# Kernel optimization log

Hardware: AMD Instinct MI355X
Metric: run time of the kernel (lower is better)

## Reference

```python
import jax, jax.numpy as jnp
import numpy as np
import math

N_HEAD = 16
ROPE_BASE = 10000.0


def _rotate_half(x):
    d2 = x.shape[-1] // 2
    return jnp.concatenate([-x[..., d2:], x[..., :d2]], axis=-1)


def _rope_sin_cos(T, d_head, dtype):
    half = d_head // 2
    inv_freq = ROPE_BASE ** (-(jnp.arange(half, dtype=dtype) / half))  # (half,)
    t = jnp.arange(T, dtype=dtype)[:, None]                            # (T,1)
    angles = t * inv_freq[None, :]                                     # (T,half)
    sin = jnp.sin(angles)
    cos = jnp.cos(angles)
    sin = jnp.concatenate([sin, sin], axis=-1)  # (T,d_head)
    cos = jnp.concatenate([cos, cos], axis=-1)
    return sin, cos


def setup_inputs() -> dict:
    key = jax.random.key(0)
    ks = jax.random.split(key, 4)
    B, T, C = 2, 2048, 1024
    x = jax.random.normal(ks[0], (B, T, C), dtype=jnp.float32)
    padding_mask = jnp.ones((B, T), dtype=bool)
    W_kqv = jax.random.normal(ks[1], (3 * C, C), dtype=jnp.float32) * (1.0 / math.sqrt(C))
    b_kqv = jnp.zeros((3 * C,), dtype=jnp.float32)
    W_proj = jax.random.normal(ks[2], (C, C), dtype=jnp.float32) * (1.0 / math.sqrt(C))
    b_proj = jnp.zeros((C,), dtype=jnp.float32)
    return {"x": x, "padding_mask": padding_mask, "W_kqv": W_kqv,
            "b_kqv": b_kqv, "W_proj": W_proj, "b_proj": b_proj}


def reference(x, padding_mask, W_kqv, b_kqv, W_proj, b_proj):
    B, T, C = x.shape
    H = N_HEAD
    D = C // H
    qkv = jnp.einsum('btc,fc->btf', x, W_kqv) + b_kqv  # (B,T,3C)
    # NOTE: original chunks as k, q, v (in that order)
    k, q, v = jnp.split(qkv, 3, axis=-1)

    def split_heads(t):
        return t.reshape(B, T, H, D).transpose(0, 2, 1, 3)  # (B,H,T,D)

    q, k, v = split_heads(q), split_heads(k), split_heads(v)

    sin, cos = _rope_sin_cos(T, D, x.dtype)  # (T,D)
    sin = sin[None, None]
    cos = cos[None, None]
    q = q * cos + _rotate_half(q) * sin
    k = k * cos + _rotate_half(k) * sin

    att = jnp.einsum('bhqd,bhkd->bhqk', q, k) * (1.0 / math.sqrt(D))  # (B,H,T,T)
    causal = jnp.tril(jnp.ones((T, T), dtype=bool))[None, None]
    att = jnp.where(causal, att, -jnp.inf)
    key_mask = padding_mask[:, None, None, :]
    att = jnp.where(key_mask, att, -jnp.inf)
    att = jax.nn.softmax(att, axis=-1)
    y = jnp.einsum('bhqk,bhkd->bhqd', att, v)  # (B,H,T,D)
    qry_mask = padding_mask[:, None, :, None].astype(y.dtype)
    y = y * qry_mask
    y = y.transpose(0, 2, 1, 3).reshape(B, T, C)
    return jnp.einsum('btc,oc->bto', y, W_proj) + b_proj
```

## Files before the change

### kernel.cpp

```cpp
#include <hip/hip_runtime.h>

typedef unsigned short u16;
typedef unsigned int   u32;
typedef __attribute__((ext_vector_type(4))) float f32x4;
typedef __attribute__((ext_vector_type(2))) float f32x2;
typedef __attribute__((ext_vector_type(8))) short short8;
typedef __attribute__((ext_vector_type(8))) unsigned short u16x8;
typedef __attribute__((ext_vector_type(4))) unsigned short u16x4;
typedef __attribute__((ext_vector_type(2))) unsigned int u32x2;

__device__ __forceinline__ u16 f2b(float f) {
  u32 u = __float_as_uint(f);
  u32 r = u + 0x7FFFu + ((u >> 16) & 1u);
  return (u16)(r >> 16);
}

__device__ __forceinline__ void gl_lds16(const void* g, void* l) {
  __builtin_amdgcn_global_load_lds((const __attribute__((address_space(1))) void*)g,
                                   (__attribute__((address_space(3))) void*)l, 16, 0, 0);
}

__global__ void cvt_all(const float* __restrict__ x, const float* __restrict__ wk,
                        const float* __restrict__ wp,
                        u16* __restrict__ xb, u16* __restrict__ wkb, u16* __restrict__ wpb,
                        float* __restrict__ cs) {
  if (blockIdx.x >= 8192) {
    const int t = (blockIdx.x - 8192) * 8 + (threadIdx.x >> 5);
    const int i = threadIdx.x & 31;
    float inv = powf(10000.0f, -((float)i) / 32.0f);
    float ang = (float)t * inv;
    f32x2 p; p[0] = cosf(ang); p[1] = sinf(ang);
    *(f32x2*)&cs[t * 64 + i * 2] = p;
    return;
  }
  int i = blockIdx.x * 256 + threadIdx.x;
  const float* s; u16* d; int off;
  if (i < 1048576)      { s = x;  d = xb;  off = i; }
  else if (i < 1835008) { s = wk; d = wkb; off = i - 1048576; }
  else                  { s = wp; d = wpb; off = i - 1835008; }
  f32x4 v = ((const f32x4*)s)[off];
  u16x4 o;
#pragma unroll
  for (int j = 0; j < 4; ++j) o[j] = f2b(v[j]);
  ((u16x4*)d)[off] = o;
}

template <int OUT_BF16>
__global__ __launch_bounds__(256, 3) void gemm_bt(
    const u16* __restrict__ A, const u16* __restrict__ Bt,
    const float* __restrict__ bias, void* __restrict__ Cv,
    int M, int N, int K) {
  __shared__ __align__(16) u16 As[128 * 64];
  __shared__ __align__(16) u16 Bs[128 * 64];
  const int tid = threadIdx.x;
  const int lane = tid & 63;
  const int w = tid >> 6;
  const int wr = w >> 1, wc = w & 1;
  const int l15 = lane & 15, l4 = lane >> 4;
  const int ntn = N >> 7;
  const int bm = blockIdx.x / ntn;
  const int bn = blockIdx.x - bm * ntn;
  const int m0 = bm << 7, n0 = bn << 7;

  int rc[4], so[4];
#pragma unroll
  for (int j = 0; j < 4; ++j) {
    const int c = tid + j * 256;
    rc[j] = c >> 3;
    so[j] = ((c & 7) ^ (rc[j] & 7)) << 3;
  }
  const int sw = l15 & 7;

  f32x4 acc[4][4] = {};

  for (int kt = 0; kt < K; kt += 64) {
    __syncthreads();
#pragma unroll
    for (int j = 0; j < 4; ++j) {
      gl_lds16(A + (size_t)(m0 + rc[j]) * K + kt + so[j], &As[(tid + j * 256) * 8]);
      gl_lds16(Bt + (size_t)(n0 + rc[j]) * K + kt + so[j], &Bs[(tid + j * 256) * 8]);
    }
    __syncthreads();
    short8 af[4][2], bf[4][2];
#pragma unroll
    for (int m = 0; m < 4; ++m)
#pragma unroll
      for (int kk = 0; kk < 2; ++kk)
        af[m][kk] = *(const short8*)&As[(wr * 64 + m * 16 + l15) * 64 + (((kk * 4 + l4) ^ sw) << 3)];
#pragma unroll
    for (int n = 0; n < 4; ++n)
#pragma unroll
      for (int kk = 0; kk < 2; ++kk)
        bf[n][kk] = *(const short8*)&Bs[(wc * 64 + n * 16 + l15) * 64 + (((kk * 4 + l4) ^ sw) << 3)];
#pragma unroll
    for (int m = 0; m < 4; ++m)
#pragma unroll
      for (int n = 0; n < 4; ++n) {
        acc[m][n] = __builtin_amdgcn_mfma_f32_16x16x32_bf16(af[m][0], bf[n][0], acc[m][n], 0, 0, 0);
        acc[m][n] = __builtin_amdgcn_mfma_f32_16x16x32_bf16(af[m][1], bf[n][1], acc[m][n], 0, 0, 0);
      }
  }

#pragma unroll
  for (int n = 0; n < 4; ++n) {
    const int col = n0 + wc * 64 + n * 16 + l15;
    const float bv = bias[col];
#pragma unroll
    for (int m = 0; m < 4; ++m) {
      const int row0 = m0 + wr * 64 + m * 16 + l4 * 4;
#pragma unroll
      for (int r = 0; r < 4; ++r) {
        float v = acc[m][n][r] + bv;
        if (OUT_BF16)
          ((u16*)Cv)[(size_t)(row0 + r) * N + col] = f2b(v);
        else
          ((float*)Cv)[(size_t)(row0 + r) * N + col] = v;
      }
    }
  }
}

__global__ __launch_bounds__(256, 3) void gemm_qkv(
    const u16* __restrict__ A, const u16* __restrict__ Bt,
    const float* __restrict__ bias, const float* __restrict__ cs,
    u16* __restrict__ qb, u16* __restrict__ kb, u16* __restrict__ vT) {
  const int K = 1024;
  __shared__ __align__(16) u16 As[128 * 64];
  __shared__ __align__(16) u16 Bs[128 * 64];
  const int tid = threadIdx.x;
  const int lane = tid & 63;
  const int w = tid >> 6;
  const int wr = w >> 1, wc = w & 1;
  const int l15 = lane & 15, l4 = lane >> 4;
  const int ntn = 24;
  const int bm = blockIdx.x / ntn;
  const int bn = blockIdx.x - bm * ntn;
  const int m0 = bm << 7, n0 = bn << 7;

  int rc[4], so[4];
#pragma unroll
  for (int j = 0; j < 4; ++j) {
    const int c = tid + j * 256;
    rc[j] = c >> 3;
    so[j] = ((c & 7) ^ (rc[j] & 7)) << 3;
  }
  const int sw = l15 & 7;

  f32x4 acc[4][4] = {};

  for (int kt = 0; kt < K; kt += 64) {
    __syncthreads();
#pragma unroll
    for (int j = 0; j < 4; ++j) {
      gl_lds16(A + (size_t)(m0 + rc[j]) * K + kt + so[j], &As[(tid + j * 256) * 8]);
      gl_lds16(Bt + (size_t)(n0 + rc[j]) * K + kt + so[j], &Bs[(tid + j * 256) * 8]);
    }
    __syncthreads();
    short8 af[4][2], bf[4][2];
#pragma unroll
    for (int m = 0; m < 4; ++m)
#pragma unroll
      for (int kk = 0; kk < 2; ++kk)
        af[m][kk] = *(const short8*)&As[(wr * 64 + m * 16 + l15) * 64 + (((kk * 4 + l4) ^ sw) << 3)];
#pragma unroll
    for (int n = 0; n < 4; ++n)
#pragma unroll
      for (int kk = 0; kk < 2; ++kk)
        bf[n][kk] = *(const short8*)&Bs[(wc * 64 + n * 16 + l15) * 64 + (((kk * 4 + l4) ^ sw) << 3)];
#pragma unroll
    for (int m = 0; m < 4; ++m)
#pragma unroll
      for (int n = 0; n < 4; ++n) {
        acc[m][n] = __builtin_amdgcn_mfma_f32_16x16x32_bf16(af[m][0], bf[n][0], acc[m][n], 0, 0, 0);
        acc[m][n] = __builtin_amdgcn_mfma_f32_16x16x32_bf16(af[m][1], bf[n][1], acc[m][n], 0, 0, 0);
      }
  }

  const int hb = bn * 2 + wc;
  const int f = hb >> 4;
  const int head = hb & 15;

  if (f == 2) {
#pragma unroll
    for (int n = 0; n < 4; ++n) {
      const int d = n * 16 + l15;
      const float bv = bias[hb * 64 + d];
#pragma unroll
      for (int m = 0; m < 4; ++m) {
        const int row = m0 + wr * 64 + m * 16 + l4 * 4;
        const int b = row >> 11, t0 = row & 2047;
        u16x4 pk;
#pragma unroll
        for (int r = 0; r < 4; ++r) pk[r] = f2b(acc[m][n][r] + bv);
        *(u16x4*)&vT[((size_t)((b * 16 + head) * 64 + d)) * 2048 + t0] = pk;
      }
    }
  } else {
    u16* const dst = (f == 1) ? qb : kb;
    const float qs = (f == 1) ? 0.180336881f : 1.0f;
#pragma unroll
    for (int n = 0; n < 2; ++n) {
      const int d = n * 16 + l15;
      const float blo = bias[hb * 64 + d];
      const float bhi = bias[hb * 64 + d + 32];
#pragma unroll
      for (int m = 0; m < 4; ++m) {
        const int row = m0 + wr * 64 + m * 16 + l4 * 4;
        const int b = row >> 11, t0 = row & 2047;
        const size_t base = ((size_t)((b * 16 + head) * 2048 + t0)) * 64 + 2 * d;
#pragma unroll
        for (int r = 0; r < 4; ++r) {
          const f32x2 csv = *(const f32x2*)&cs[(size_t)(t0 + r) * 64 + d * 2];
          const float lo = acc[m][n][r] + blo;
          const float hi = acc[m][n + 2][r] + bhi;
          const float olo = (lo * csv[0] - hi * csv[1]) * qs;
          const float ohi = (hi * csv[0] + lo * csv[1]) * qs;
          u32 pw;
          asm("v_cvt_pk_bf16_f32 %0, %1, %2" : "=v"(pw) : "v"(olo), "v"(ohi));
          *(u32*)&dst[base + (size_t)r * 64] = pw;
        }
      }
    }
  }
}

__device__ __forceinline__ void attn9_step(
    const u16* __restrict__ Kp, const u16* __restrict__ Vp,
    u32* __restrict__ P, int kv0, int q0w, bool masked, int l15, int l4,
    const short8& qf0, const short8& qf1, f32x4 (&acc)[4], float& rs) {
  f32x4 st[4];
  __builtin_amdgcn_s_setprio(1);
#pragma unroll
  for (int nb = 0; nb < 4; ++nb) {
    const int rr = nb * 16 + l15;
    const int e0 = (l4 ^ (rr & 7)) << 3;
    const int e1 = ((l4 + 4) ^ (rr & 7)) << 3;
    const short8 k0 = *(const short8*)&Kp[rr * 64 + e0];
    const short8 k1 = *(const short8*)&Kp[rr * 64 + e1];
    f32x4 a = {};
    a = __builtin_amdgcn_mfma_f32_16x16x32_bf16(k0, qf0, a, 0, 0, 0);
    a = __builtin_amdgcn_mfma_f32_16x16x32_bf16(k1, qf1, a, 0, 0, 0);
    st[nb] = a;
  }
  __builtin_amdgcn_s_setprio(0);
  const int qq = q0w + l15;
  float rsl = 0.f;
#pragma unroll
  for (int nb = 0; nb < 4; ++nb) {
    float p[4];
#pragma unroll
    for (int r = 0; r < 4; ++r) {
      float s = st[nb][r];
      const int kk = kv0 + nb * 16 + l4 * 4 + r;
      s = (masked && (kk > qq)) ? -1e30f : s;
      asm("v_exp_f32 %0, %1" : "=v"(p[r]) : "v"(s));
      rsl += p[r];
    }
    u32x2 pw;
    asm("v_cvt_pk_bf16_f32 %0, %1, %2" : "=v"(pw[0]) : "v"(p[0]), "v"(p[1]));
    asm("v_cvt_pk_bf16_f32 %0, %1, %2" : "=v"(pw[1]) : "v"(p[2]), "v"(p[3]));
    *(u32x2*)&P[l15 * 36 + nb * 8 + l4 * 2] = pw;
  }
  rs += rsl;
  const short8 pa0 = *(const short8*)&P[l15 * 36 + l4 * 4];
  const short8 pa1 = *(const short8*)&P[l15 * 36 + 16 + l4 * 4];
  __builtin_amdgcn_s_setprio(1);
#pragma unroll
  for (int dnb = 0; dnb < 4; ++dnb) {
    const int rr = dnb * 16 + l15;
    const int e0 = (l4 ^ (rr & 7)) << 3;
    const int e1 = ((l4 + 4) ^ (rr & 7)) << 3;
    const short8 v0 = *(const short8*)&Vp[rr * 64 + e0];
    const short8 v1 = *(const short8*)&Vp[rr * 64 + e1];
    acc[dnb] = __builtin_amdgcn_mfma_f32_16x16x32_bf16(pa0, v0, acc[dnb], 0, 0, 0);
    acc[dnb] = __builtin_amdgcn_mfma_f32_16x16x32_bf16(pa1, v1, acc[dnb], 0, 0, 0);
  }
  __builtin_amdgcn_s_setprio(0);
}

__global__ __launch_bounds__(256, 3) void attn9(
    const u16* __restrict__ qb, const u16* __restrict__ kb,
    const u16* __restrict__ vT, u16* __restrict__ yb) {
  __shared__ __align__(16) u16 Ks[2][64 * 64];
  __shared__ __align__(16) u16 Vs[2][64 * 64];
  __shared__ __align__(16) u32 Psm[4][16 * 36];
  const int tid = threadIdx.x;
  const int lane = tid & 63;
  const int w = tid >> 6;
  const int l15 = lane & 15, l4 = lane >> 4;
  const int bh = blockIdx.x & 31;
  const int qi = 31 - (blockIdx.x >> 5);
  const int b = bh >> 4, head = bh & 15;
  const int p0 = qi * 64;
  const int nst = qi + 1;
  const int q0w = p0 + w * 16;

  const u16* qbase = qb + (size_t)bh * 2048 * 64;
  const u16* kbase = kb + (size_t)bh * 2048 * 64;
  const u16* vbase = vT + (size_t)bh * 64 * 2048;
  u32* const P = &Psm[w][0];

  const int r0 = tid >> 3, c0 = tid & 7;
  const int r1 = (tid + 256) >> 3, c1 = tid & 7;
  const int sc0 = ((c0 ^ (r0 & 7)) << 3);
  const int sc1 = ((c1 ^ (r1 & 7)) << 3);
  u16* const Kd0 = &Ks[0][tid * 8];        u16* const Kd0b = &Ks[0][(tid + 256) * 8];
  u16* const Kd1 = &Ks[1][tid * 8];        u16* const Kd1b = &Ks[1][(tid + 256) * 8];
  u16* const Vd0 = &Vs[0][tid * 8];        u16* const Vd0b = &Vs[0][(tid + 256) * 8];
  u16* const Vd1 = &Vs[1][tid * 8];        u16* const Vd1b = &Vs[1][(tid + 256) * 8];

#define STAGE(BUF, KV0)                                                        \
  do {                                                                         \
    const int _kv = (KV0);                                                     \
    gl_lds16(kbase + (size_t)(_kv + r0) * 64 + sc0, (BUF) ? Kd1 : Kd0);        \
    gl_lds16(kbase + (size_t)(_kv + r1) * 64 + sc1, (BUF) ? Kd1b : Kd0b);      \
    gl_lds16(vbase + (size_t)r0 * 2048 + _kv + sc0, (BUF) ? Vd1 : Vd0);        \
    gl_lds16(vbase + (size_t)r1 * 2048 + _kv + sc1, (BUF) ? Vd1b : Vd0b);      \
  } while (0)

  const short8 qf0 = *(const short8*)&qbase[(size_t)(q0w + l15) * 64 + l4 * 8];
  const short8 qf1 = *(const short8*)&qbase[(size_t)(q0w + l15) * 64 + 32 + l4 * 8];
  f32x4 acc[4] = {};
  float rs = 0.f;

  int cur = 0;
  STAGE(0, 0);
  for (int t = 0; t < nst; ++t) {
    __syncthreads();
    if (t + 1 < nst) STAGE(cur ^ 1, (t + 1) * 64);
    attn9_step(&Ks[cur][0], &Vs[cur][0], P, t * 64, q0w, t == nst - 1,
               l15, l4, qf0, qf1, acc, rs);
    cur ^= 1;
  }
#undef STAGE

  float rsum = rs;
  rsum += __shfl_xor(rsum, 16);
  rsum += __shfl_xor(rsum, 32);
  float linv[4];
#pragma unroll
  for (int r = 0; r < 4; ++r) linv[r] = 1.f / __shfl(rsum, l4 * 4 + r);
#pragma unroll
  for (int dnb = 0; dnb < 4; ++dnb) {
    const int col = head * 64 + dnb * 16 + l15;
#pragma unroll
    for (int r = 0; r < 4; ++r) {
      const int q = q0w + l4 * 4 + r;
      yb[((size_t)(b * 2048 + q)) * 1024 + col] = f2b(acc[dnb][r] * linv[r]);
    }
  }
}

extern "C" void kernel_launch(void* const* d_in, const int* in_sizes, int n_in,
                              void* d_out, int out_size, void* d_ws, size_t ws_size,
                              hipStream_t stream) {
  const float* x = (const float*)d_in[0];
  const float* W_kqv = (const float*)d_in[2];
  const float* b_kqv = (const float*)d_in[3];
  const float* W_proj = (const float*)d_in[4];
  const float* b_proj = (const float*)d_in[5];
  float* out = (float*)d_out;
  char* ws = (char*)d_ws;
  const size_t MB = (size_t)1 << 20;
  u16* xb = (u16*)(ws + 0);
  u16* wkb = (u16*)(ws + 8 * MB);
  u16* wpb = (u16*)(ws + 14 * MB);
  u16* qb = (u16*)(ws + 40 * MB);
  u16* kb = (u16*)(ws + 48 * MB);
  u16* vTb = (u16*)(ws + 56 * MB);
  u16* yb = (u16*)(ws + 64 * MB);
  float* cs = (float*)(ws + 72 * MB);

  cvt_all<<<8448, 256, 0, stream>>>(x, W_kqv, W_proj, xb, wkb, wpb, cs);
  gemm_qkv<<<768, 256, 0, stream>>>(xb, wkb, b_kqv, cs, qb, kb, vTb);
  attn9<<<1024, 256, 0, stream>>>(qb, kb, vTb, yb);
  gemm_bt<0><<<256, 256, 0, stream>>>(yb, wpb, b_proj, out, 4096, 1024, 1024);
}
```

Before: 104.2 us.

## Process two query sub-tiles per wave in attention, halving waves per block

The attention kernel now uses 2 waves per block instead of 4, and each wave handles 32 query rows as two 16-row halves. Each K/V fragment read from shared memory is reused for both halves, which halves LDS read traffic per MFMA. The cost is more registers per wave, fewer waves per block to hide latency, and each thread issuing twice as many global-to-LDS copies per stage.

```diff
diff --git a/kernel.cpp b/kernel.cpp
--- a/kernel.cpp
+++ b/kernel.cpp
@@ -224,11 +224,12 @@
   }
 }
 
-__device__ __forceinline__ void attn9_step(
+__device__ __forceinline__ void attn10_step(
     const u16* __restrict__ Kp, const u16* __restrict__ Vp,
-    u32* __restrict__ P, int kv0, int q0w, bool masked, int l15, int l4,
-    const short8& qf0, const short8& qf1, f32x4 (&acc)[4], float& rs) {
-  f32x4 st[4];
+    u32* __restrict__ P0, u32* __restrict__ P1,
+    int kv0, int q0w, bool masked, int l15, int l4,
+    const short8 (&qf)[2][2], f32x4 (&acc)[2][4], float (&rs)[2]) {
+  f32x4 st[2][4];
   __builtin_amdgcn_s_setprio(1);
 #pragma unroll
   for (int nb = 0; nb < 4; ++nb) {
@@ -237,33 +238,42 @@
     const int e1 = ((l4 + 4) ^ (rr & 7)) << 3;
     const short8 k0 = *(const short8*)&Kp[rr * 64 + e0];
     const short8 k1 = *(const short8*)&Kp[rr * 64 + e1];
-    f32x4 a = {};
-    a = __builtin_amdgcn_mfma_f32_16x16x32_bf16(k0, qf0, a, 0, 0, 0);
-    a = __builtin_amdgcn_mfma_f32_16x16x32_bf16(k1, qf1, a, 0, 0, 0);
-    st[nb] = a;
+    f32x4 a0 = {}, a1 = {};
+    a0 = __builtin_amdgcn_mfma_f32_16x16x32_bf16(k0, qf[0][0], a0, 0, 0, 0);
+    a0 = __builtin_amdgcn_mfma_f32_16x16x32_bf16(k1, qf[0][1], a0, 0, 0, 0);
+    a1 = __builtin_amdgcn_mfma_f32_16x16x32_bf16(k0, qf[1][0], a1, 0, 0, 0);
+    a1 = __builtin_amdgcn_mfma_f32_16x16x32_bf16(k1, qf[1][1], a1, 0, 0, 0);
+    st[0][nb] = a0;
+    st[1][nb] = a1;
   }
   __builtin_amdgcn_s_setprio(0);
-  const int qq = q0w + l15;
-  float rsl = 0.f;
-#pragma unroll
-  for (int nb = 0; nb < 4; ++nb) {
-    float p[4];
-#pragma unroll
-    for (int r = 0; r < 4; ++r) {
-      float s = st[nb][r];
-      const int kk = kv0 + nb * 16 + l4 * 4 + r;
-      s = (masked && (kk > qq)) ? -1e30f : s;
-      asm("v_exp_f32 %0, %1" : "=v"(p[r]) : "v"(s));
-      rsl += p[r];
-    }
-    u32x2 pw;
-    asm("v_cvt_pk_bf16_f32 %0, %1, %2" : "=v"(pw[0]) : "v"(p[0]), "v"(p[1]));
-    asm("v_cvt_pk_bf16_f32 %0, %1, %2" : "=v"(pw[1]) : "v"(p[2]), "v"(p[3]));
-    *(u32x2*)&P[l15 * 36 + nb * 8 + l4 * 2] = pw;
-  }
-  rs += rsl;
-  const short8 pa0 = *(const short8*)&P[l15 * 36 + l4 * 4];
-  const short8 pa1 = *(const short8*)&P[l15 * 36 + 16 + l4 * 4];
+#pragma unroll
+  for (int h = 0; h < 2; ++h) {
+    u32* const P = h ? P1 : P0;
+    const int qq = q0w + h * 16 + l15;
+    float rsl = 0.f;
+#pragma unroll
+    for (int nb = 0; nb < 4; ++nb) {
+      float p[4];
+#pragma unroll
+      for (int r = 0; r < 4; ++r) {
+        float s = st[h][nb][r];
+        const int kk = kv0 + nb * 16 + l4 * 4 + r;
+        s = (masked && (kk > qq)) ? -1e30f : s;
+        asm("v_exp_f32 %0, %1" : "=v"(p[r]) : "v"(s));
+        rsl += p[r];
+      }
+      u32x2 pw;
+      asm("v_cvt_pk_bf16_f32 %0, %1, %2" : "=v"(pw[0]) : "v"(p[0]), "v"(p[1]));
+      asm("v_cvt_pk_bf16_f32 %0, %1, %2" : "=v"(pw[1]) : "v"(p[2]), "v"(p[3]));
+      *(u32x2*)&P[l15 * 36 + nb * 8 + l4 * 2] = pw;
+    }
+    rs[h] += rsl;
+  }
+  const short8 pa00 = *(const short8*)&P0[l15 * 36 + l4 * 4];
+  const short8 pa01 = *(const short8*)&P0[l15 * 36 + 16 + l4 * 4];
+  const short8 pa10 = *(const short8*)&P1[l15 * 36 + l4 * 4];
+  const short8 pa11 = *(const short8*)&P1[l15 * 36 + 16 + l4 * 4];
   __builtin_amdgcn_s_setprio(1);
 #pragma unroll
   for (int dnb = 0; dnb < 4; ++dnb) {
@@ -272,18 +282,20 @@
     const int e1 = ((l4 + 4) ^ (rr & 7)) << 3;
     const short8 v0 = *(const short8*)&Vp[rr * 64 + e0];
     const short8 v1 = *(const short8*)&Vp[rr * 64 + e1];
-    acc[dnb] = __builtin_amdgcn_mfma_f32_16x16x32_bf16(pa0, v0, acc[dnb], 0, 0, 0);
-    acc[dnb] = __builtin_amdgcn_mfma_f32_16x16x32_bf16(pa1, v1, acc[dnb], 0, 0, 0);
+    acc[0][dnb] = __builtin_amdgcn_mfma_f32_16x16x32_bf16(pa00, v0, acc[0][dnb], 0, 0, 0);
+    acc[0][dnb] = __builtin_amdgcn_mfma_f32_16x16x32_bf16(pa01, v1, acc[0][dnb], 0, 0, 0);
+    acc[1][dnb] = __builtin_amdgcn_mfma_f32_16x16x32_bf16(pa10, v0, acc[1][dnb], 0, 0, 0);
+    acc[1][dnb] = __builtin_amdgcn_mfma_f32_16x16x32_bf16(pa11, v1, acc[1][dnb], 0, 0, 0);
   }
   __builtin_amdgcn_s_setprio(0);
 }
 
-__global__ __launch_bounds__(256, 3) void attn9(
+__global__ __launch_bounds__(128, 2) void attn10(
     const u16* __restrict__ qb, const u16* __restrict__ kb,
     const u16* __restrict__ vT, u16* __restrict__ yb) {
   __shared__ __align__(16) u16 Ks[2][64 * 64];
   __shared__ __align__(16) u16 Vs[2][64 * 64];
-  __shared__ __align__(16) u32 Psm[4][16 * 36];
+  __shared__ __align__(16) u32 Psm[2][2][16 * 36];
   const int tid = threadIdx.x;
   const int lane = tid & 63;
   const int w = tid >> 6;
@@ -293,60 +305,68 @@
   const int b = bh >> 4, head = bh & 15;
   const int p0 = qi * 64;
   const int nst = qi + 1;
-  const int q0w = p0 + w * 16;
+  const int q0w = p0 + w * 32;
 
   const u16* qbase = qb + (size_t)bh * 2048 * 64;
   const u16* kbase = kb + (size_t)bh * 2048 * 64;
   const u16* vbase = vT + (size_t)bh * 64 * 2048;
-  u32* const P = &Psm[w][0];
-
-  const int r0 = tid >> 3, c0 = tid & 7;
-  const int r1 = (tid + 256) >> 3, c1 = tid & 7;
-  const int sc0 = ((c0 ^ (r0 & 7)) << 3);
-  const int sc1 = ((c1 ^ (r1 & 7)) << 3);
-  u16* const Kd0 = &Ks[0][tid * 8];        u16* const Kd0b = &Ks[0][(tid + 256) * 8];
-  u16* const Kd1 = &Ks[1][tid * 8];        u16* const Kd1b = &Ks[1][(tid + 256) * 8];
-  u16* const Vd0 = &Vs[0][tid * 8];        u16* const Vd0b = &Vs[0][(tid + 256) * 8];
-  u16* const Vd1 = &Vs[1][tid * 8];        u16* const Vd1b = &Vs[1][(tid + 256) * 8];
-
-#define STAGE(BUF, KV0)                                                        \
-  do {                                                                         \
-    const int _kv = (KV0);                                                     \
-    gl_lds16(kbase + (size_t)(_kv + r0) * 64 + sc0, (BUF) ? Kd1 : Kd0);        \
-    gl_lds16(kbase + (size_t)(_kv + r1) * 64 + sc1, (BUF) ? Kd1b : Kd0b);      \
-    gl_lds16(vbase + (size_t)r0 * 2048 + _kv + sc0, (BUF) ? Vd1 : Vd0);        \
-    gl_lds16(vbase + (size_t)r1 * 2048 + _kv + sc1, (BUF) ? Vd1b : Vd0b);      \
+  u32* const P0 = &Psm[w][0][0];
+  u32* const P1 = &Psm[w][1][0];
+
+  int rc[4], sc[4];
+#pragma unroll
+  for (int j = 0; j < 4; ++j) {
+    const int c = tid + j * 128;
+    rc[j] = c >> 3;
+    sc[j] = ((c & 7) ^ (rc[j] & 7)) << 3;
+  }
+
+#define STAGE(BUF, KV0)                                                         \
+  do {                                                                          \
+    const int _kv = (KV0);                                                      \
+    _Pragma("unroll")                                                           \
+    for (int j = 0; j < 4; ++j) {                                               \
+      gl_lds16(kbase + (size_t)(_kv + rc[j]) * 64 + sc[j], &Ks[BUF][(tid + j * 128) * 8]); \
+      gl_lds16(vbase + (size_t)rc[j] * 2048 + _kv + sc[j], &Vs[BUF][(tid + j * 128) * 8]); \
+    }                                                                           \
   } while (0)
 
-  const short8 qf0 = *(const short8*)&qbase[(size_t)(q0w + l15) * 64 + l4 * 8];
-  const short8 qf1 = *(const short8*)&qbase[(size_t)(q0w + l15) * 64 + 32 + l4 * 8];
-  f32x4 acc[4] = {};
-  float rs = 0.f;
+  short8 qf[2][2];
+#pragma unroll
+  for (int h = 0; h < 2; ++h) {
+    qf[h][0] = *(const short8*)&qbase[(size_t)(q0w + h * 16 + l15) * 64 + l4 * 8];
+    qf[h][1] = *(const short8*)&qbase[(size_t)(q0w + h * 16 + l15) * 64 + 32 + l4 * 8];
+  }
+  f32x4 acc[2][4] = {};
+  float rs[2] = {0.f, 0.f};
 
   int cur = 0;
   STAGE(0, 0);
   for (int t = 0; t < nst; ++t) {
     __syncthreads();
     if (t + 1 < nst) STAGE(cur ^ 1, (t + 1) * 64);
-    attn9_step(&Ks[cur][0], &Vs[cur][0], P, t * 64, q0w, t == nst - 1,
-               l15, l4, qf0, qf1, acc, rs);
+    attn10_step(&Ks[cur][0], &Vs[cur][0], P0, P1, t * 64, q0w, t == nst - 1,
+                l15, l4, qf, acc, rs);
     cur ^= 1;
   }
 #undef STAGE
 
-  float rsum = rs;
-  rsum += __shfl_xor(rsum, 16);
-  rsum += __shfl_xor(rsum, 32);
-  float linv[4];
-#pragma unroll
-  for (int r = 0; r < 4; ++r) linv[r] = 1.f / __shfl(rsum, l4 * 4 + r);
-#pragma unroll
-  for (int dnb = 0; dnb < 4; ++dnb) {
-    const int col = head * 64 + dnb * 16 + l15;
-#pragma unroll
-    for (int r = 0; r < 4; ++r) {
-      const int q = q0w + l4 * 4 + r;
-      yb[((size_t)(b * 2048 + q)) * 1024 + col] = f2b(acc[dnb][r] * linv[r]);
+#pragma unroll
+  for (int h = 0; h < 2; ++h) {
+    float rsum = rs[h];
+    rsum += __shfl_xor(rsum, 16);
+    rsum += __shfl_xor(rsum, 32);
+    float linv[4];
+#pragma unroll
+    for (int r = 0; r < 4; ++r) linv[r] = 1.f / __shfl(rsum, l4 * 4 + r);
+#pragma unroll
+    for (int dnb = 0; dnb < 4; ++dnb) {
+      const int col = head * 64 + dnb * 16 + l15;
+#pragma unroll
+      for (int r = 0; r < 4; ++r) {
+        const int q = q0w + h * 16 + l4 * 4 + r;
+        yb[((size_t)(b * 2048 + q)) * 1024 + col] = f2b(acc[h][dnb][r] * linv[r]);
+      }
     }
   }
 }
@@ -373,6 +393,6 @@
 
   cvt_all<<<8448, 256, 0, stream>>>(x, W_kqv, W_proj, xb, wkb, wpb, cs);
   gemm_qkv<<<768, 256, 0, stream>>>(xb, wkb, b_kqv, cs, qb, kb, vTb);
-  attn9<<<1024, 256, 0, stream>>>(qb, kb, vTb, yb);
+  attn10<<<1024, 128, 0, stream>>>(qb, kb, vTb, yb);
   gemm_bt<0><<<256, 256, 0, stream>>>(yb, wpb, b_proj, out, 4096, 1024, 1024);
 }
```

Result: slower. 111.2 us (+6.8%).
